# Performance work log

Measured on AMD Instinct MI355X. Metric: run time of the kernel, lower is better.

The kernel has to match this reference:

```python
import jax, jax.numpy as jnp
import numpy as np

B, T, D, F, C = 16384, 256, 8, 512, 16  # batch, trees, depth, features, classes
L = 2 ** D  # leaves per tree


def setup_inputs() -> dict:
    key = jax.random.key(0)
    k1, k2, k3, k4 = jax.random.split(key, 4)
    x = jax.random.normal(k1, (B, F), dtype=jnp.float32)
    feature_weights = jax.random.normal(k2, (T, D, F), dtype=jnp.float32)
    thresholds = jax.random.normal(k3, (T, D), dtype=jnp.float32)
    responses = jax.random.normal(k4, (T, L, C), dtype=jnp.float32)
    return {"x": x, "feature_weights": feature_weights,
            "thresholds": thresholds, "responses": responses}


def reference(x, feature_weights, thresholds, responses):
    # Hard feature selection per (tree, level): argmax over features.
    fidx = jnp.argmax(feature_weights, axis=-1)            # [T, D] int
    fv = x[:, fidx]                                        # [B, T, D] gather
    bits = (fv > thresholds[None, :, :]).astype(x.dtype)   # [B, T, D]
    # decision = sum_d bit_d * 2^(D-1-d)  (matches decision*2+bit loop)
    powers = (2 ** jnp.arange(D - 1, -1, -1)).astype(x.dtype)  # [D]
    decision = jnp.sum(bits * powers, axis=-1).astype(jnp.int32)  # [B, T]
    # Gather leaf responses per (sample, tree) and average over trees.
    tree_ids = jnp.arange(T)[None, :]                      # [1, T]
    leaf_out = responses[tree_ids, decision]               # [B, T, C]
    out = jnp.mean(leaf_out, axis=1)                       # [B, C]
    return out  # dropout is identity at eval time
```

## Files before the change

### kernel.cpp

```cpp
#include <hip/hip_runtime.h>

constexpr int B = 16384;
constexpr int T = 256;
constexpr int D = 8;
constexpr int F = 512;
constexpr int C = 16;
constexpr int L = 256;

struct FP { int fidx; float thr; };

__global__ __launch_bounds__(256) void node_prep_kernel(
    const float* __restrict__ fw,
    const float* __restrict__ thr,
    FP* __restrict__ packed)
{
    const int wave = threadIdx.x >> 6;
    const int lane = threadIdx.x & 63;
    const int row  = blockIdx.x * 4 + wave;
    const float* base = fw + (size_t)row * F;

    float best = -INFINITY;
    int bidx = 0;
#pragma unroll
    for (int k = 0; k < F / 64; ++k) {
        const int idx = lane + k * 64;
        const float v = base[idx];
        if (v > best) { best = v; bidx = idx; }
    }
#pragma unroll
    for (int off = 32; off >= 1; off >>= 1) {
        const float ov = __shfl_xor(best, off);
        const int   oi = __shfl_xor(bidx, off);
        if (ov > best || (ov == best && oi < bidx)) { best = ov; bidx = oi; }
    }
    if (lane == 0) {
        FP p;
        p.fidx = bidx;
        p.thr  = thr[row];
        packed[row] = p;
    }
}

__global__ __launch_bounds__(256) void forest_kernel(
    const float* __restrict__ x,
    const FP* __restrict__ packed,
    const float* __restrict__ responses,
    float* __restrict__ out)
{
    __shared__ float xrow[F];
    __shared__ int   sdec[T];
    __shared__ float sacc[16][16];

    const int b   = blockIdx.x;
    const int tid = threadIdx.x;

    const float2 v2 = reinterpret_cast<const float2*>(x + (size_t)b * F)[tid];
    xrow[tid * 2]     = v2.x;
    xrow[tid * 2 + 1] = v2.y;
    __syncthreads();

    const int2* p2 = reinterpret_cast<const int2*>(packed) + tid * D;
    int2 raw[D];
#pragma unroll
    for (int d = 0; d < D; ++d) raw[d] = p2[d];
    int dec = 0;
#pragma unroll
    for (int d = 0; d < D; ++d) {
        const float fv = xrow[raw[d].x];
        const float th = __int_as_float(raw[d].y);
        dec |= (fv > th) ? (128 >> d) : 0;
    }
    sdec[tid] = dec;
    __syncthreads();

    const int g = tid >> 4;
    const int c = tid & 15;
    float acc = 0.0f;
#pragma unroll
    for (int k = 0; k < 16; ++k) {
        const int t  = g * 16 + k;
        const int dd = sdec[t];
        acc += responses[(size_t)((t << 8) | dd) * C + c];
    }
    sacc[g][c] = acc;
    __syncthreads();

    if (tid < 16) {
        float s = 0.0f;
#pragma unroll
        for (int gg = 0; gg < 16; ++gg) s += sacc[gg][tid];
        out[(size_t)b * C + tid] = s * (1.0f / T);
    }
}

extern "C" void kernel_launch(void* const* d_in, const int* in_sizes, int n_in,
                              void* d_out, int out_size, void* d_ws, size_t ws_size,
                              hipStream_t stream) {
    const float* x         = (const float*)d_in[0];
    const float* fw        = (const float*)d_in[1];
    const float* thr       = (const float*)d_in[2];
    const float* responses = (const float*)d_in[3];
    float* out             = (float*)d_out;

    FP* packed = (FP*)d_ws;

    node_prep_kernel<<<(T * D) / 4, 256, 0, stream>>>(fw, thr, packed);
    forest_kernel<<<B, 256, 0, stream>>>(x, packed, responses, out);
}
```

Before: 113.9 us.

## Process four samples per block and reduce leaf gathers with wave shuffles

Each block now handles four samples. The per-thread packed node data (feature index and threshold) is loaded once and reused across all four samples. The leaf-response gather is restructured so each wave owns one sample: decisions are stored as bytes, read as int4 words, and accumulated into two independent accumulators. A shuffle-based reduction within the wave replaces the shared-memory reduction and its extra barrier. This cuts redundant packed-node loads and launch/sync overhead, at the cost of more shared memory per block and four times fewer blocks.

```diff
diff --git a/kernel.cpp b/kernel.cpp
--- a/kernel.cpp
+++ b/kernel.cpp
@@ -47,50 +47,74 @@
     const float* __restrict__ responses,
     float* __restrict__ out)
 {
-    __shared__ float xrow[F];
-    __shared__ int   sdec[T];
-    __shared__ float sacc[16][16];
+    __shared__ float xrow[4][F];
+    __shared__ unsigned char sdec[4][T];
 
-    const int b   = blockIdx.x;
+    const int b0  = blockIdx.x * 4;
     const int tid = threadIdx.x;
 
-    const float2 v2 = reinterpret_cast<const float2*>(x + (size_t)b * F)[tid];
-    xrow[tid * 2]     = v2.x;
-    xrow[tid * 2 + 1] = v2.y;
+    {
+        const float4* xs = reinterpret_cast<const float4*>(x + (size_t)b0 * F);
+        float4* xl = reinterpret_cast<float4*>(&xrow[0][0]);
+        xl[tid]       = xs[tid];
+        xl[tid + 256] = xs[tid + 256];
+    }
     __syncthreads();
 
-    const int2* p2 = reinterpret_cast<const int2*>(packed) + tid * D;
-    int2 raw[D];
+    {
+        const int2* p2 = reinterpret_cast<const int2*>(packed) + tid * D;
+        int2 raw[D];
 #pragma unroll
-    for (int d = 0; d < D; ++d) raw[d] = p2[d];
-    int dec = 0;
+        for (int d = 0; d < D; ++d) raw[d] = p2[d];
+        int dec0 = 0, dec1 = 0, dec2 = 0, dec3 = 0;
 #pragma unroll
-    for (int d = 0; d < D; ++d) {
-        const float fv = xrow[raw[d].x];
-        const float th = __int_as_float(raw[d].y);
-        dec |= (fv > th) ? (128 >> d) : 0;
+        for (int d = 0; d < D; ++d) {
+            const int   f  = raw[d].x;
+            const float th = __int_as_float(raw[d].y);
+            const int   p  = 128 >> d;
+            dec0 |= (xrow[0][f] > th) ? p : 0;
+            dec1 |= (xrow[1][f] > th) ? p : 0;
+            dec2 |= (xrow[2][f] > th) ? p : 0;
+            dec3 |= (xrow[3][f] > th) ? p : 0;
+        }
+        sdec[0][tid] = (unsigned char)dec0;
+        sdec[1][tid] = (unsigned char)dec1;
+        sdec[2][tid] = (unsigned char)dec2;
+        sdec[3][tid] = (unsigned char)dec3;
     }
-    sdec[tid] = dec;
     __syncthreads();
 
-    const int g = tid >> 4;
-    const int c = tid & 15;
-    float acc = 0.0f;
+    const int w    = tid >> 6;
+    const int lane = tid & 63;
+    const int slot = lane >> 4;
+    const int c    = lane & 15;
+    const int sh   = slot * 8;
+
+    float accA = 0.0f, accB = 0.0f;
+    const int4* pdec = reinterpret_cast<const int4*>(&sdec[w][0]);
+
+#define GATH(ACC, WD, TB)                                                  \
+    {                                                                      \
+        const int dd = ((WD) >> sh) & 255;                                 \
+        const int t  = (TB) + slot;                                        \
+        ACC += responses[((size_t)(((t) << 8) | dd) << 4) + c];            \
+    }
+
 #pragma unroll
-    for (int k = 0; k < 16; ++k) {
-        const int t  = g * 16 + k;
-        const int dd = sdec[t];
-        acc += responses[(size_t)((t << 8) | dd) * C + c];
+    for (int kk = 0; kk < 16; ++kk) {
+        const int4 pd = pdec[kk];
+        GATH(accA, pd.x, kk * 16 + 0)
+        GATH(accB, pd.y, kk * 16 + 4)
+        GATH(accA, pd.z, kk * 16 + 8)
+        GATH(accB, pd.w, kk * 16 + 12)
     }
-    sacc[g][c] = acc;
-    __syncthreads();
+#undef GATH
 
-    if (tid < 16) {
-        float s = 0.0f;
-#pragma unroll
-        for (int gg = 0; gg < 16; ++gg) s += sacc[gg][tid];
-        out[(size_t)b * C + tid] = s * (1.0f / T);
-    }
+    float acc = accA + accB;
+    acc += __shfl_xor(acc, 16);
+    acc += __shfl_xor(acc, 32);
+
+    if (lane < 16) out[(size_t)(b0 + w) * C + lane] = acc * (1.0f / T);
 }
 
 extern "C" void kernel_launch(void* const* d_in, const int* in_sizes, int n_in,
@@ -105,5 +129,5 @@
     FP* packed = (FP*)d_ws;
 
     node_prep_kernel<<<(T * D) / 4, 256, 0, stream>>>(fw, thr, packed);
-    forest_kernel<<<B, 256, 0, stream>>>(x, packed, responses, out);
+    forest_kernel<<<B / 4, 256, 0, stream>>>(x, packed, responses, out);
 }
```

New measurement: 125.4 us. +10.1%, slower.
